# Optimization experiments

Measured on AMD Instinct MI355X. Metric: run time of the kernel, lower is better.

## Reference

```python
import jax, jax.numpy as jnp
import numpy as np

IN_F = 256
OUT_F = 256
H = 4
HD = OUT_F // H  # 64
N = 20000
E = 160000
B = 1
LN_EPS = 1e-5
NEG_SLOPE = 0.2


def setup_inputs() -> dict:
    key = jax.random.key(0)
    k1, k2, k3, k4 = jax.random.split(key, 4)
    node_features = jax.random.normal(k1, (B, N, IN_F), dtype=jnp.float32)
    edge_index = jax.random.randint(k2, (2, E), 0, N, dtype=jnp.int64)
    # per-head linear weights, stacked: [H, IN_F, HD]
    W = jax.random.normal(k3, (H, IN_F, HD), dtype=jnp.float32) / np.sqrt(IN_F)
    # per-head attention vectors on concat([src, dst]): [H, 2*HD]
    a = jax.random.normal(k4, (H, 2 * HD), dtype=jnp.float32) / np.sqrt(2 * HD)
    gamma = jnp.ones((OUT_F,), dtype=jnp.float32)
    beta = jnp.zeros((OUT_F,), dtype=jnp.float32)
    return {"node_features": node_features, "edge_index": edge_index,
            "W": W, "a": a, "gamma": gamma, "beta": beta}


def reference(node_features, edge_index, W, a, gamma, beta):
    src_idx, dst_idx = edge_index[0], edge_index[1]
    # per-head linear transform: [B, H, N, HD]
    t = jnp.einsum('bnf,hfd->bhnd', node_features, W)
    # gather edge endpoints: [B, H, E, HD]
    src = t[:, :, src_idx, :]
    dst = t[:, :, dst_idx, :]
    # attention score = a . concat(src, dst), split a into halves
    scores = (jnp.einsum('bhed,hd->bhe', src, a[:, :HD]) +
              jnp.einsum('bhed,hd->bhe', dst, a[:, HD:]))
    scores = jnp.where(scores >= 0, scores, NEG_SLOPE * scores)
    # NOTE: faithful to the original — softmax over ALL edges (dim=-1), not per-destination
    w = jax.nn.softmax(scores, axis=-1)  # [B, H, E]
    # scatter-add weighted src features into destination nodes
    agg = jnp.zeros_like(t).at[:, :, dst_idx, :].add(w[..., None] * src)  # [B, H, N, HD]
    # concat heads (head-major, matching torch.cat over head_outputs)
    out = agg.transpose(0, 2, 1, 3).reshape(B, N, OUT_F)
    # LayerNorm
    mean = out.mean(-1, keepdims=True)
    var = out.var(-1, keepdims=True)
    out = (out - mean) / jnp.sqrt(var + LN_EPS) * gamma + beta
    return out
```

## Files before the change

### kernel.cpp

```cpp
#include <hip/hip_runtime.h>

#define IN_F   256
#define OUT_F  256
#define NHEAD  4
#define HD     64
#define NN     20000
#define NE     160000
#define LN_EPS 1e-5f
#define SLOPE  0.2f
#define BUCKET 64

typedef __attribute__((ext_vector_type(8))) short short8;
typedef __attribute__((ext_vector_type(4))) float f32x4;

__device__ __forceinline__ unsigned short rne_bf16(float f) {
  unsigned u = __float_as_uint(f);
  u += 0x7FFFu + ((u >> 16) & 1u);
  return (unsigned short)(u >> 16);
}
__device__ __forceinline__ float bf2f(unsigned short u) {
  return __uint_as_float((unsigned)u << 16);
}
__device__ __forceinline__ unsigned pk2(float lo, float hi) {
  return (unsigned)rne_bf16(lo) | ((unsigned)rne_bf16(hi) << 16);
}

__global__ __launch_bounds__(256) void conv_w(const float* __restrict__ W,
                                              unsigned short* __restrict__ Wt,
                                              int* __restrict__ deg) {
  int i = blockIdx.x * 256 + threadIdx.x;
  if (i < NN) deg[i] = 0;
  if (i < 16384) {
    int fq  = i & 63;
    int col = i >> 6;
    int h = col >> 6, d = col & 63;
    const float* src = W + ((size_t)h * IN_F + fq * 4) * HD + d;
    ushort4 o;
    o.x = rne_bf16(src[0]);
    o.y = rne_bf16(src[64]);
    o.z = rne_bf16(src[128]);
    o.w = rne_bf16(src[192]);
    *reinterpret_cast<ushort4*>(Wt + (size_t)col * IN_F + fq * 4) = o;
  }
}

__global__ __launch_bounds__(256) void gemm_mfma(const float* __restrict__ X,
                                                 const unsigned short* __restrict__ Wt,
                                                 const float* __restrict__ a,
                                                 unsigned short* __restrict__ Tb,
                                                 float* __restrict__ asrc,
                                                 float* __restrict__ adst) {
  __shared__ unsigned Alds[64 * 32];
  __shared__ unsigned Blds[256 * 32];
  const int tid  = threadIdx.x;
  const int lane = tid & 63;
  const int wid  = tid >> 6;
  const int row0 = blockIdx.x * 64;

  f32x4 acc[4][4];
  #pragma unroll
  for (int r = 0; r < 4; ++r)
    #pragma unroll
    for (int c = 0; c < 4; ++c) acc[r][c] = (f32x4){0.f, 0.f, 0.f, 0.f};

  const int ar = tid >> 2;
  const int aq = tid & 3;
  const int s0 = (aq * 2) ^ (ar & 7);
  const int s1 = (aq * 2 + 1) ^ (ar & 7);
  const bool aok = (row0 + ar) < NN;
  const float* xrow = X + (size_t)(row0 + ar) * IN_F + aq * 16;

  for (int kt = 0; kt < 4; ++kt) {
    const int k0 = kt * 64;
    if (kt) __syncthreads();
    float4 x0 = {0,0,0,0}, x1 = {0,0,0,0}, x2 = {0,0,0,0}, x3 = {0,0,0,0};
    if (aok) {
      const float4* xp = reinterpret_cast<const float4*>(xrow + k0);
      x0 = xp[0]; x1 = xp[1]; x2 = xp[2]; x3 = xp[3];
    }
    uint4 U0 = {pk2(x0.x,x0.y), pk2(x0.z,x0.w), pk2(x1.x,x1.y), pk2(x1.z,x1.w)};
    uint4 U1 = {pk2(x2.x,x2.y), pk2(x2.z,x2.w), pk2(x3.x,x3.y), pk2(x3.z,x3.w)};
    *reinterpret_cast<uint4*>(&Alds[ar * 32 + s0 * 4]) = U0;
    *reinterpret_cast<uint4*>(&Alds[ar * 32 + s1 * 4]) = U1;
    #pragma unroll
    for (int i = 0; i < 8; ++i) {
      int c   = wid * 8 + i;
      int col = c * 8 + (lane >> 3);
      int kch = (lane & 7) ^ (col & 7);
      const unsigned short* src = Wt + (size_t)col * IN_F + k0 + kch * 8;
      __builtin_amdgcn_global_load_lds(
          (const __attribute__((address_space(1))) void*)src,
          (__attribute__((address_space(3))) void*)((char*)Blds + c * 1024),
          16, 0, 0);
    }
    __syncthreads();
    const int g = lane >> 4;
    #pragma unroll
    for (int kf = 0; kf < 2; ++kf) {
      short8 afr[4], bfr[4];
      #pragma unroll
      for (int r = 0; r < 4; ++r) {
        int row  = 16 * r + (lane & 15);
        int slot = (4 * kf + g) ^ (row & 7);
        afr[r] = *reinterpret_cast<const short8*>(&Alds[row * 32 + slot * 4]);
      }
      #pragma unroll
      for (int c = 0; c < 4; ++c) {
        int col  = wid * 64 + 16 * c + (lane & 15);
        int slot = (4 * kf + g) ^ (col & 7);
        bfr[c] = *reinterpret_cast<const short8*>(&Blds[col * 32 + slot * 4]);
      }
      #pragma unroll
      for (int r = 0; r < 4; ++r)
        #pragma unroll
        for (int c = 0; c < 4; ++c)
          acc[r][c] = __builtin_amdgcn_mfma_f32_16x16x32_bf16(afr[r], bfr[c], acc[r][c], 0, 0, 0);
    }
  }

  const int g  = lane >> 4;
  const int lc = lane & 15;
  float as_[4], ad_[4];
  #pragma unroll
  for (int fc = 0; fc < 4; ++fc) {
    as_[fc] = a[wid * 128 + fc * 16 + lc];
    ad_[fc] = a[wid * 128 + 64 + fc * 16 + lc];
  }
  #pragma unroll
  for (int r = 0; r < 4; ++r) {
    #pragma unroll
    for (int reg = 0; reg < 4; ++reg) {
      int row = row0 + 16 * r + g * 4 + reg;
      float ps = 0.f, pd = 0.f;
      if (row < NN) {
        #pragma unroll
        for (int fc = 0; fc < 4; ++fc) {
          float v = acc[r][fc][reg];
          ps = fmaf(v, as_[fc], ps);
          pd = fmaf(v, ad_[fc], pd);
          Tb[(size_t)row * OUT_F + wid * 64 + fc * 16 + lc] = rne_bf16(v);
        }
      }
      #pragma unroll
      for (int off = 1; off < 16; off <<= 1) {
        ps += __shfl_xor(ps, off, 64);
        pd += __shfl_xor(pd, off, 64);
      }
      if (lc == 0 && row < NN) {
        asrc[row * 4 + wid] = ps;
        adst[row * 4 + wid] = pd;
      }
    }
  }
}

__global__ __launch_bounds__(256) void score_exp_fill(const int* __restrict__ ei,
                                                      const float* __restrict__ asrc,
                                                      const float* __restrict__ adst,
                                                      float* __restrict__ expb,
                                                      float* __restrict__ partials,
                                                      int* __restrict__ deg,
                                                      int2* __restrict__ pairs) {
  __shared__ float red[4][4];
  const int tid  = threadIdx.x;
  const int lane = tid & 63;
  const int wid  = tid >> 6;
  const int e = blockIdx.x * 256 + tid;

  int s = ei[e], t = ei[NE + e];
  float4 av = reinterpret_cast<const float4*>(asrc)[s];
  float4 dv = reinterpret_cast<const float4*>(adst)[t];
  float sc[4] = {av.x + dv.x, av.y + dv.y, av.z + dv.z, av.w + dv.w};
  float ex[4];
  #pragma unroll
  for (int h = 0; h < 4; ++h) {
    sc[h] = sc[h] >= 0.f ? sc[h] : SLOPE * sc[h];
    ex[h] = expf(sc[h]);
  }
  reinterpret_cast<float4*>(expb)[e] = make_float4(ex[0], ex[1], ex[2], ex[3]);
  int pos = atomicAdd(&deg[t], 1);
  pairs[(size_t)t * BUCKET + pos] = make_int2(s, e);

  #pragma unroll
  for (int off = 1; off < 64; off <<= 1) {
    #pragma unroll
    for (int h = 0; h < 4; ++h) ex[h] += __shfl_xor(ex[h], off, 64);
  }
  if (lane == 0) {
    #pragma unroll
    for (int h = 0; h < 4; ++h) red[wid][h] = ex[h];
  }
  __syncthreads();
  if (tid < 4)
    partials[blockIdx.x * 4 + tid] = red[0][tid] + red[1][tid] + red[2][tid] + red[3][tid];
}

__global__ __launch_bounds__(1024) void sumexp_reduce(const float* __restrict__ partials,
                                                      float* __restrict__ sumexp) {
  __shared__ float psum[16][4];
  const int tid  = threadIdx.x;
  const int lane = tid & 63;
  const int wid  = tid >> 6;
  float v = partials[tid] + partials[tid + 1024];
  if (tid + 2048 < 2500) v += partials[tid + 2048];
  #pragma unroll
  for (int off = 4; off < 64; off <<= 1) v += __shfl_xor(v, off, 64);
  if (lane < 4) psum[wid][lane] = v;
  __syncthreads();
  if (tid < 4) {
    float s = 0.f;
    #pragma unroll
    for (int w = 0; w < 16; ++w) s += psum[w][tid];
    sumexp[tid] = s;
  }
}

__global__ __launch_bounds__(256) void agg_ln_kernel(const int* __restrict__ deg,
                                                     const int2* __restrict__ pairs,
                                                     const float* __restrict__ expb,
                                                     const float* __restrict__ sumexp,
                                                     const unsigned short* __restrict__ Tb,
                                                     const float* __restrict__ gamma,
                                                     const float* __restrict__ beta,
                                                     float* __restrict__ out) {
  int n = (blockIdx.x * blockDim.x + threadIdx.x) >> 6;
  int lane = threadIdx.x & 63;
  if (n >= NN) return;
  int h = lane >> 4;
  float rs = 1.0f / sumexp[h];
  int d = deg[n];
  const int2* bp = pairs + (size_t)n * BUCKET;
  float4 acc = make_float4(0.f, 0.f, 0.f, 0.f);
  const ushort4* T4 = reinterpret_cast<const ushort4*>(Tb);
  for (int p = 0; p < d; ++p) {
    int2 se = bp[p];
    float w = expb[se.y * 4 + h] * rs;
    ushort4 v = T4[(size_t)se.x * 64 + lane];
    acc.x = fmaf(w, bf2f(v.x), acc.x);
    acc.y = fmaf(w, bf2f(v.y), acc.y);
    acc.z = fmaf(w, bf2f(v.z), acc.z);
    acc.w = fmaf(w, bf2f(v.w), acc.w);
  }
  float s = acc.x + acc.y + acc.z + acc.w;
  float q = acc.x * acc.x + acc.y * acc.y + acc.z * acc.z + acc.w * acc.w;
  #pragma unroll
  for (int off = 1; off < 64; off <<= 1) {
    s += __shfl_xor(s, off, 64);
    q += __shfl_xor(q, off, 64);
  }
  float mean = s * (1.f / 256.f);
  float var  = q * (1.f / 256.f) - mean * mean;
  float rstd = rsqrtf(var + LN_EPS);
  float4 g = reinterpret_cast<const float4*>(gamma)[lane];
  float4 b = reinterpret_cast<const float4*>(beta)[lane];
  float4 o;
  o.x = (acc.x - mean) * rstd * g.x + b.x;
  o.y = (acc.y - mean) * rstd * g.y + b.y;
  o.z = (acc.z - mean) * rstd * g.z + b.z;
  o.w = (acc.w - mean) * rstd * g.w + b.w;
  reinterpret_cast<float4*>(out)[(size_t)n * 64 + lane] = o;
}

extern "C" void kernel_launch(void* const* d_in, const int* in_sizes, int n_in,
                              void* d_out, int out_size, void* d_ws, size_t ws_size,
                              hipStream_t stream) {
  const float* X     = (const float*)d_in[0];
  const int*   ei    = (const int*)d_in[1];
  const float* W     = (const float*)d_in[2];
  const float* a     = (const float*)d_in[3];
  const float* gamma = (const float*)d_in[4];
  const float* beta  = (const float*)d_in[5];
  float* out = (float*)d_out;

  float* ws = (float*)d_ws;
  const size_t OFF_STATS  = 0;
  const size_t OFF_DEG    = 16;
  const size_t OFF_PART   = OFF_DEG + NN;
  const size_t OFF_PAIRS  = OFF_PART + 2560;
  const size_t OFF_WT     = OFF_PAIRS + (size_t)NN * BUCKET * 2;
  const size_t OFF_T      = OFF_WT + 32768;
  const size_t OFF_ASRC   = OFF_T + (size_t)NN * 128;
  const size_t OFF_ADST   = OFF_ASRC + NN * 4;
  const size_t OFF_EXPB   = OFF_ADST + NN * 4;

  float*          sumexp   = ws + OFF_STATS;
  int*            deg      = (int*)(ws + OFF_DEG);
  float*          partials = ws + OFF_PART;
  int2*           pairs    = (int2*)(ws + OFF_PAIRS);
  unsigned short* Wt       = (unsigned short*)(ws + OFF_WT);
  unsigned short* Tb       = (unsigned short*)(ws + OFF_T);
  float*          asrc     = ws + OFF_ASRC;
  float*          adst     = ws + OFF_ADST;
  float*          expb     = ws + OFF_EXPB;

  conv_w<<<80, 256, 0, stream>>>(W, Wt, deg);
  gemm_mfma<<<(NN + 63) / 64, 256, 0, stream>>>(X, Wt, a, Tb, asrc, adst);
  score_exp_fill<<<NE / 256, 256, 0, stream>>>(ei, asrc, adst, expb, partials, deg, pairs);
  sumexp_reduce<<<1, 1024, 0, stream>>>(partials, sumexp);
  agg_ln_kernel<<<(NN + 3) / 4, 256, 0, stream>>>(deg, pairs, expb, sumexp, Tb,
                                                  gamma, beta, out);
}
```

Measured before the change: 68.27 us.

## Fuse sumexp reduction into score kernel via last-block pattern, unroll aggregation

```diff
diff --git a/kernel.cpp b/kernel.cpp
--- a/kernel.cpp
+++ b/kernel.cpp
@@ -9,6 +9,7 @@
 #define LN_EPS 1e-5f
 #define SLOPE  0.2f
 #define BUCKET 64
+#define SE_GRID (NE / 256)
 
 typedef __attribute__((ext_vector_type(8))) short short8;
 typedef __attribute__((ext_vector_type(4))) float f32x4;
@@ -27,9 +28,11 @@
 
 __global__ __launch_bounds__(256) void conv_w(const float* __restrict__ W,
                                               unsigned short* __restrict__ Wt,
-                                              int* __restrict__ deg) {
+                                              int* __restrict__ deg,
+                                              int* __restrict__ counter) {
   int i = blockIdx.x * 256 + threadIdx.x;
   if (i < NN) deg[i] = 0;
+  if (i == 0) *counter = 0;
   if (i < 16384) {
     int fq  = i & 63;
     int col = i >> 6;
@@ -160,8 +163,11 @@
                                                       float* __restrict__ expb,
                                                       float* __restrict__ partials,
                                                       int* __restrict__ deg,
-                                                      int2* __restrict__ pairs) {
+                                                      int2* __restrict__ pairs,
+                                                      float* __restrict__ sumexp,
+                                                      int* __restrict__ counter) {
   __shared__ float red[4][4];
+  __shared__ int amLast;
   const int tid  = threadIdx.x;
   const int lane = tid & 63;
   const int wid  = tid >> 6;
@@ -193,25 +199,25 @@
   __syncthreads();
   if (tid < 4)
     partials[blockIdx.x * 4 + tid] = red[0][tid] + red[1][tid] + red[2][tid] + red[3][tid];
-}
-
-__global__ __launch_bounds__(1024) void sumexp_reduce(const float* __restrict__ partials,
-                                                      float* __restrict__ sumexp) {
-  __shared__ float psum[16][4];
-  const int tid  = threadIdx.x;
-  const int lane = tid & 63;
-  const int wid  = tid >> 6;
-  float v = partials[tid] + partials[tid + 1024];
-  if (tid + 2048 < 2500) v += partials[tid + 2048];
-  #pragma unroll
-  for (int off = 4; off < 64; off <<= 1) v += __shfl_xor(v, off, 64);
-  if (lane < 4) psum[wid][lane] = v;
   __syncthreads();
-  if (tid < 4) {
-    float s = 0.f;
-    #pragma unroll
-    for (int w = 0; w < 16; ++w) s += psum[w][tid];
-    sumexp[tid] = s;
+
+  if (tid == 0) {
+    __threadfence();
+    int prev = atomicAdd(counter, 1);
+    amLast = (prev == SE_GRID - 1);
+  }
+  __syncthreads();
+  if (amLast) {
+    __threadfence();
+    float v = 0.f;
+    for (int i = tid; i < SE_GRID * 4; i += 256)
+      v += ((volatile const float*)partials)[i];
+    #pragma unroll
+    for (int off = 4; off < 64; off <<= 1) v += __shfl_xor(v, off, 64);
+    if (lane < 4) red[wid][lane] = v;
+    __syncthreads();
+    if (tid < 4) sumexp[tid] = red[0][tid] + red[1][tid] + red[2][tid] + red[3][tid];
+    if (tid == 0) *counter = 0;
   }
 }
 
@@ -227,20 +233,35 @@
   int lane = threadIdx.x & 63;
   if (n >= NN) return;
   int h = lane >> 4;
-  float rs = 1.0f / sumexp[h];
   int d = deg[n];
-  const int2* bp = pairs + (size_t)n * BUCKET;
+  const int2* bp  = pairs + (size_t)n * BUCKET;
+  const int4* bp2 = reinterpret_cast<const int4*>(bp);
   float4 acc = make_float4(0.f, 0.f, 0.f, 0.f);
   const ushort4* T4 = reinterpret_cast<const ushort4*>(Tb);
-  for (int p = 0; p < d; ++p) {
+  int p = 0;
+  for (; p + 2 <= d; p += 2) {
+    int4 two = bp2[p >> 1];
+    float w0 = expb[two.y * 4 + h];
+    float w1 = expb[two.w * 4 + h];
+    ushort4 v0 = T4[(size_t)two.x * 64 + lane];
+    ushort4 v1 = T4[(size_t)two.z * 64 + lane];
+    acc.x = fmaf(w1, bf2f(v1.x), fmaf(w0, bf2f(v0.x), acc.x));
+    acc.y = fmaf(w1, bf2f(v1.y), fmaf(w0, bf2f(v0.y), acc.y));
+    acc.z = fmaf(w1, bf2f(v1.z), fmaf(w0, bf2f(v0.z), acc.z));
+    acc.w = fmaf(w1, bf2f(v1.w), fmaf(w0, bf2f(v0.w), acc.w));
+  }
+  if (p < d) {
     int2 se = bp[p];
-    float w = expb[se.y * 4 + h] * rs;
+    float w = expb[se.y * 4 + h];
     ushort4 v = T4[(size_t)se.x * 64 + lane];
     acc.x = fmaf(w, bf2f(v.x), acc.x);
     acc.y = fmaf(w, bf2f(v.y), acc.y);
     acc.z = fmaf(w, bf2f(v.z), acc.z);
     acc.w = fmaf(w, bf2f(v.w), acc.w);
   }
+  float rs = 1.0f / sumexp[h];
+  acc.x *= rs; acc.y *= rs; acc.z *= rs; acc.w *= rs;
+
   float s = acc.x + acc.y + acc.z + acc.w;
   float q = acc.x * acc.x + acc.y * acc.y + acc.z * acc.z + acc.w * acc.w;
   #pragma unroll
@@ -284,6 +305,7 @@
   const size_t OFF_EXPB   = OFF_ADST + NN * 4;
 
   float*          sumexp   = ws + OFF_STATS;
+  int*            counter  = (int*)(ws + OFF_STATS + 8);
   int*            deg      = (int*)(ws + OFF_DEG);
   float*          partials = ws + OFF_PART;
   int2*           pairs    = (int2*)(ws + OFF_PAIRS);
@@ -293,10 +315,10 @@
   float*          adst     = ws + OFF_ADST;
   float*          expb     = ws + OFF_EXPB;
 
-  conv_w<<<80, 256, 0, stream>>>(W, Wt, deg);
+  conv_w<<<80, 256, 0, stream>>>(W, Wt, deg, counter);
   gemm_mfma<<<(NN + 63) / 64, 256, 0, stream>>>(X, Wt, a, Tb, asrc, adst);
-  score_exp_fill<<<NE / 256, 256, 0, stream>>>(ei, asrc, adst, expb, partials, deg, pairs);
-  sumexp_reduce<<<1, 1024, 0, stream>>>(partials, sumexp);
+  score_exp_fill<<<SE_GRID, 256, 0, stream>>>(ei, asrc, adst, expb, partials, deg,
+                                              pairs, sumexp, counter);
   agg_ln_kernel<<<(NN + 3) / 4, 256, 0, stream>>>(deg, pairs, expb, sumexp, Tb,
                                                   gamma, beta, out);
 }
```

Measured after the change: 87.96 us. +28.8%, slower.
